# Optimization experiments

Hardware: AMD Instinct MI355X
Metric: run time of the kernel (lower is better)

## Reference

```python
import jax, jax.numpy as jnp
import numpy as np
from jax import lax

B, N, H, L, K = 16, 2000, 128, 3, 5
LN_EPS = 1e-5


def setup_inputs() -> dict:
    key = jax.random.key(0)
    ks = jax.random.split(key, 4)
    node_emb = jax.random.normal(ks[0], (B, N, H), dtype=jnp.float32)
    dist_matrix = jax.random.uniform(ks[1], (B, N, N), dtype=jnp.float32)
    Ws = jax.random.normal(ks[2], (L, H, H), dtype=jnp.float32) / np.sqrt(H)
    bs = jax.random.normal(ks[3], (L, H), dtype=jnp.float32) * 0.02
    gammas = jnp.ones((L, H), dtype=jnp.float32)
    betas = jnp.zeros((L, H), dtype=jnp.float32)
    return {"node_emb": node_emb, "dist_matrix": dist_matrix,
            "Ws": Ws, "bs": bs, "gammas": gammas, "betas": betas}


def _layer_norm(x, gamma, beta):
    mu = jnp.mean(x, axis=-1, keepdims=True)
    var = jnp.mean(jnp.square(x - mu), axis=-1, keepdims=True)
    return (x - mu) * lax.rsqrt(var + LN_EPS) * gamma + beta


def reference(node_emb, dist_matrix, Ws, bs, gammas, betas):
    # kNN mask: k smallest distances per row (B, N, K)
    _, knn_idx = lax.top_k(-dist_matrix, K)
    b_ix = jnp.arange(B)[:, None, None]
    n_ix = jnp.arange(N)[None, :, None]
    knn_mask = jnp.zeros((B, N, N), dtype=bool).at[b_ix, n_ix, knn_idx].set(True)
    scores = jnp.where(knn_mask, -dist_matrix, -jnp.inf)
    weights = jax.nn.softmax(scores, axis=-1)  # (B, N, N)

    h = node_emb
    for l in range(L):
        agg = jnp.einsum('bnm,bmh->bnh', weights, h)
        delta = jax.nn.relu(agg @ Ws[l].T + bs[l])
        h = _layer_norm(h + delta, gammas[l], betas[l])
    return h
```

## Files before the change

### kernel.cpp

```cpp
#include <hip/hip_runtime.h>
#include <hip/hip_bf16.h>

#define BATCH 16
#define NNODE 2000
#define HDIM  128
#define KNN   5
#define NROWS (BATCH * NNODE)
#define LN_EPS 1e-5f

typedef __attribute__((ext_vector_type(8))) short short8;
typedef __attribute__((ext_vector_type(4))) float f32x4;

__device__ __forceinline__ float b2f(short s) {
    unsigned int u = ((unsigned int)(unsigned short)s) << 16;
    return __uint_as_float(u);
}
__device__ __forceinline__ short f2b(float f) {
    __hip_bfloat16 h = __float2bfloat16(f);
    return *reinterpret_cast<short*>(&h);
}

__device__ __forceinline__ unsigned long long pack_di(float v, unsigned int idx) {
    unsigned int b = __float_as_uint(v);
    b = (b & 0x80000000u) ? ~b : (b | 0x80000000u);
    return ((unsigned long long)b << 32) | idx;
}

__global__ __launch_bounds__(256) void knn_prep_kernel(
    const float* __restrict__ dist,
    const float* __restrict__ Ws,
    const float* __restrict__ node_emb,
    __hip_bfloat16* __restrict__ WB,
    short* __restrict__ hb,
    int* __restrict__ w_idx,
    float* __restrict__ w_val)
{
    int tg = blockIdx.x * 256 + threadIdx.x;

    if (tg < 3 * 2048) {
        int l    = tg >> 11;
        int r    = tg & 2047;
        int lane = r & 63;
        int ks   = (r >> 6) & 3;
        int ct   = (r >> 8) & 1;
        int wv   = (r >> 9) & 3;
        int col  = wv * 32 + ct * 16 + (lane & 15);
        int k0   = ks * 32 + (lane >> 4) * 8;
        const float* src = Ws + ((size_t)l << 14) + col * HDIM + k0;
        __hip_bfloat16* dst = WB + ((size_t)tg << 3);
        #pragma unroll
        for (int e = 0; e < 8; ++e) dst[e] = __float2bfloat16(src[e]);
    }

    if (tg < NROWS * HDIM / 8) {
        const float4* src = reinterpret_cast<const float4*>(node_emb) + tg * 2;
        float4 a = src[0], bq = src[1];
        short8 pk;
        pk[0]=f2b(a.x); pk[1]=f2b(a.y); pk[2]=f2b(a.z); pk[3]=f2b(a.w);
        pk[4]=f2b(bq.x); pk[5]=f2b(bq.y); pk[6]=f2b(bq.z); pk[7]=f2b(bq.w);
        *reinterpret_cast<short8*>(hb + (size_t)tg * 8) = pk;
    }

    int row  = blockIdx.x * 4 + (threadIdx.x >> 6);
    int lane = threadIdx.x & 63;
    const float4* r4 = reinterpret_cast<const float4*>(dist + (size_t)row * NNODE);

    unsigned long long pk0 = ~0ull, pk1 = ~0ull, pk2 = ~0ull, pk3 = ~0ull, pk4 = ~0ull;

    auto ins = [&](float d, int m) {
        unsigned long long key = pack_di(d, (unsigned int)m);
        if (key < pk4) {
            pk4 = key;
            unsigned long long t;
            if (pk4 < pk3) { t = pk3; pk3 = pk4; pk4 = t; }
            if (pk3 < pk2) { t = pk2; pk2 = pk3; pk3 = t; }
            if (pk2 < pk1) { t = pk1; pk1 = pk2; pk2 = t; }
            if (pk1 < pk0) { t = pk0; pk0 = pk1; pk1 = t; }
        }
    };

    float4 v[8];
    int base7 = lane + 448;
    bool has8 = base7 < (NNODE / 4);
    #pragma unroll
    for (int i = 0; i < 7; ++i) v[i] = r4[lane + 64 * i];
    v[7] = r4[has8 ? base7 : lane];

    #pragma unroll
    for (int i = 0; i < 7; ++i) {
        int base = (lane + 64 * i) * 4;
        ins(v[i].x, base); ins(v[i].y, base + 1);
        ins(v[i].z, base + 2); ins(v[i].w, base + 3);
    }
    if (has8) {
        int base = base7 * 4;
        ins(v[7].x, base); ins(v[7].y, base + 1);
        ins(v[7].z, base + 2); ins(v[7].w, base + 3);
    }

    unsigned long long chosen[KNN];
    #pragma unroll
    for (int r = 0; r < KNN; ++r) {
        unsigned long long mn = pk0;
        #pragma unroll
        for (int off = 32; off; off >>= 1) {
            unsigned long long o = __shfl_xor(mn, off, 64);
            if (o < mn) mn = o;
        }
        if (pk0 == mn) { pk0 = pk1; pk1 = pk2; pk2 = pk3; pk3 = pk4; pk4 = ~0ull; }
        chosen[r] = mn;
    }

    if (lane == 0) {
        float d[KNN]; int ix[KNN];
        #pragma unroll
        for (int r = 0; r < KNN; ++r) {
            unsigned int ub = (unsigned int)(chosen[r] >> 32);
            ub = (ub & 0x80000000u) ? (ub ^ 0x80000000u) : ~ub;
            d[r]  = __uint_as_float(ub);
            ix[r] = (int)(chosen[r] & 0xffffffffu);
        }
        float e[KNN]; float sum = 0.f;
        #pragma unroll
        for (int r = 0; r < KNN; ++r) { e[r] = expf(d[0] - d[r]); sum += e[r]; }
        float inv = 1.f / sum;
        #pragma unroll
        for (int r = 0; r < KNN; ++r) {
            w_idx[row * KNN + r] = ix[r];
            w_val[row * KNN + r] = e[r] * inv;
        }
    }
}

template<bool OUT_F32>
__global__ __launch_bounds__(256) void layer_kernel_b(
    const short* __restrict__ hin,
    const int*   __restrict__ w_idx,
    const float* __restrict__ w_val,
    const __hip_bfloat16* __restrict__ WB,
    const float* __restrict__ bias,
    const float* __restrict__ gamma,
    const float* __restrict__ beta,
    short* __restrict__ hout_b,
    float* __restrict__ hout_f)
{
    __shared__ __hip_bfloat16 aggb[16][HDIM];
    __shared__ short hown[16][HDIM];
    __shared__ int   sidx[16][KNN];
    __shared__ float sw[16][KNN];
    __shared__ float wred[4][16][2];

    int tid = threadIdx.x;
    int wv  = tid >> 6;
    int l   = tid & 63;

    int bid = blockIdx.x;
    int x   = bid & 7;
    int j   = bid >> 3;
    int hi  = (j >= 125);
    int bsw = 2 * x + hi;
    int gid = bsw * 125 + (j - hi * 125);

    int node0 = gid * 16;
    size_t hbase = (size_t)bsw * NNODE * HDIM;

    const short8* wb = reinterpret_cast<const short8*>(WB);
    short8 bfrag[2][4];
    #pragma unroll
    for (int ct = 0; ct < 2; ++ct)
        #pragma unroll
        for (int ks = 0; ks < 4; ++ks)
            bfrag[ct][ks] = wb[((wv * 2 + ct) * 4 + ks) * 64 + l];

    if (tid < 16 * KNN) {
        int m = tid / KNN, k = tid % KNN;
        sidx[m][k] = w_idx[(node0 + m) * KNN + k];
        sw[m][k]   = w_val[(node0 + m) * KNN + k];
    }
    __syncthreads();

    {
        int m  = tid >> 4;
        int c0 = (tid & 15) * 8;
        short8 own = *reinterpret_cast<const short8*>(
            hin + (size_t)(node0 + m) * HDIM + c0);
        *reinterpret_cast<short8*>(&hown[m][c0]) = own;

        float a0=0,a1=0,a2=0,a3=0,a4=0,a5=0,a6=0,a7=0;
        #pragma unroll
        for (int k = 0; k < KNN; ++k) {
            float wk = sw[m][k];
            short8 hv = *reinterpret_cast<const short8*>(
                hin + hbase + (size_t)sidx[m][k] * HDIM + c0);
            a0 = fmaf(wk, b2f(hv[0]), a0); a1 = fmaf(wk, b2f(hv[1]), a1);
            a2 = fmaf(wk, b2f(hv[2]), a2); a3 = fmaf(wk, b2f(hv[3]), a3);
            a4 = fmaf(wk, b2f(hv[4]), a4); a5 = fmaf(wk, b2f(hv[5]), a5);
            a6 = fmaf(wk, b2f(hv[6]), a6); a7 = fmaf(wk, b2f(hv[7]), a7);
        }
        short8 pk;
        pk[0]=f2b(a0); pk[1]=f2b(a1); pk[2]=f2b(a2); pk[3]=f2b(a3);
        pk[4]=f2b(a4); pk[5]=f2b(a5); pk[6]=f2b(a6); pk[7]=f2b(a7);
        *reinterpret_cast<short8*>(&aggb[tid >> 4][c0]) = pk;
    }
    __syncthreads();

    f32x4 acc0 = {0.f,0.f,0.f,0.f}, acc1 = {0.f,0.f,0.f,0.f};
    #pragma unroll
    for (int ks = 0; ks < 4; ++ks) {
        short8 afrag = *reinterpret_cast<const short8*>(&aggb[l & 15][ks * 32 + (l >> 4) * 8]);
        acc0 = __builtin_amdgcn_mfma_f32_16x16x32_bf16(afrag, bfrag[0][ks], acc0, 0, 0, 0);
        acc1 = __builtin_amdgcn_mfma_f32_16x16x32_bf16(afrag, bfrag[1][ks], acc1, 0, 0, 0);
    }

    int g = l >> 4;
    int col0 = wv * 32 + (l & 15);
    int col1 = col0 + 16;
    float b0  = bias[col0],  b1  = bias[col1];
    float gm0 = gamma[col0], gm1 = gamma[col1];
    float bt0 = beta[col0],  bt1 = beta[col1];

    float y0[4], y1[4];
    #pragma unroll
    for (int r = 0; r < 4; ++r) {
        int rl = g * 4 + r;
        y0[r] = b2f(hown[rl][col0]) + fmaxf(acc0[r] + b0, 0.f);
        y1[r] = b2f(hown[rl][col1]) + fmaxf(acc1[r] + b1, 0.f);
    }

    #pragma unroll
    for (int r = 0; r < 4; ++r) {
        float ss = y0[r] + y1[r];
        float qq = y0[r] * y0[r] + y1[r] * y1[r];
        #pragma unroll
        for (int off = 1; off < 16; off <<= 1) {
            ss += __shfl_xor(ss, off, 64);
            qq += __shfl_xor(qq, off, 64);
        }
        if ((l & 15) == 0) { wred[wv][g * 4 + r][0] = ss; wred[wv][g * 4 + r][1] = qq; }
    }
    __syncthreads();

    #pragma unroll
    for (int r = 0; r < 4; ++r) {
        int row = g * 4 + r;
        float S = wred[0][row][0] + wred[1][row][0] + wred[2][row][0] + wred[3][row][0];
        float Q = wred[0][row][1] + wred[1][row][1] + wred[2][row][1] + wred[3][row][1];
        float mu  = S * (1.f / 128.f);
        float var = Q * (1.f / 128.f) - mu * mu;
        float rs  = rsqrtf(var + LN_EPS);
        size_t orow = (size_t)(node0 + row) * HDIM;
        float o0 = (y0[r] - mu) * rs * gm0 + bt0;
        float o1 = (y1[r] - mu) * rs * gm1 + bt1;
        if (OUT_F32) {
            hout_f[orow + col0] = o0;
            hout_f[orow + col1] = o1;
        } else {
            hout_b[orow + col0] = f2b(o0);
            hout_b[orow + col1] = f2b(o1);
        }
    }
}

extern "C" void kernel_launch(void* const* d_in, const int* in_sizes, int n_in,
                              void* d_out, int out_size, void* d_ws, size_t ws_size,
                              hipStream_t stream) {
    const float* node_emb = (const float*)d_in[0];
    const float* dist     = (const float*)d_in[1];
    const float* Ws       = (const float*)d_in[2];
    const float* bs       = (const float*)d_in[3];
    const float* gammas   = (const float*)d_in[4];
    const float* betas    = (const float*)d_in[5];
    float* out = (float*)d_out;

    char* ws = (char*)d_ws;
    int*   w_idx = (int*)  (ws + 0);
    float* w_val = (float*)(ws + 640000);
    __hip_bfloat16* WB = (__hip_bfloat16*)(ws + 1280000);
    short* hb  = (short*)(ws + 1378304);
    short* h1b = (short*)(ws + 9570304);
    short* h2b = (short*)(ws + 17762304);

    knn_prep_kernel<<<NROWS / 4, 256, 0, stream>>>(
        dist, Ws, node_emb, WB, hb, w_idx, w_val);

    const int nblocks = NROWS / 16;
    const int WL = 16384;

    layer_kernel_b<false><<<nblocks, 256, 0, stream>>>(hb,  w_idx, w_val,
        WB,        bs,          gammas,          betas,          h1b, nullptr);
    layer_kernel_b<false><<<nblocks, 256, 0, stream>>>(h1b, w_idx, w_val,
        WB + WL,   bs + HDIM,   gammas + HDIM,   betas + HDIM,   h2b, nullptr);
    layer_kernel_b<true><<<nblocks, 256, 0, stream>>>(h2b, w_idx, w_val,
        WB + 2*WL, bs + 2*HDIM, gammas + 2*HDIM, betas + 2*HDIM, nullptr, out);
}
```

Measured before the change: 102.3 us.

## Fuse three layer launches into one persistent kernel with grid barrier

Replaces the three per-layer kernel launches with a single persistent kernel of fixed grid size that loops over tiles and synchronises layers through an atomic global barrier. The counters are reset in the prep kernel. This is meant to remove launch overhead and inter-kernel gaps. In exchange it lowers parallelism per layer, adds spin-wait cost, and relies on all blocks being co-resident.

```diff
diff --git a/kernel.cpp b/kernel.cpp
--- a/kernel.cpp
+++ b/kernel.cpp
@@ -6,6 +6,8 @@
 #define HDIM  128
 #define KNN   5
 #define NROWS (BATCH * NNODE)
+#define NTILE (NROWS / 16)
+#define LGRID 768
 #define LN_EPS 1e-5f
 
 typedef __attribute__((ext_vector_type(8))) short short8;
@@ -33,9 +35,15 @@
     __hip_bfloat16* __restrict__ WB,
     short* __restrict__ hb,
     int* __restrict__ w_idx,
-    float* __restrict__ w_val)
+    float* __restrict__ w_val,
+    unsigned int* __restrict__ barrier_ctr)
 {
     int tg = blockIdx.x * 256 + threadIdx.x;
+
+    if (tg < 4) {
+        __hip_atomic_store(&barrier_ctr[tg], 0u, __ATOMIC_RELAXED,
+                           __HIP_MEMORY_SCOPE_AGENT);
+    }
 
     if (tg < 3 * 2048) {
         int l    = tg >> 11;
@@ -132,17 +140,18 @@
     }
 }
 
-template<bool OUT_F32>
-__global__ __launch_bounds__(256) void layer_kernel_b(
-    const short* __restrict__ hin,
+__global__ __launch_bounds__(256, 4) void gcn_layers_kernel(
+    const short* __restrict__ hb,
     const int*   __restrict__ w_idx,
     const float* __restrict__ w_val,
     const __hip_bfloat16* __restrict__ WB,
-    const float* __restrict__ bias,
-    const float* __restrict__ gamma,
-    const float* __restrict__ beta,
-    short* __restrict__ hout_b,
-    float* __restrict__ hout_f)
+    const float* __restrict__ bs,
+    const float* __restrict__ gammas,
+    const float* __restrict__ betas,
+    short* __restrict__ h1b,
+    short* __restrict__ h2b,
+    float* __restrict__ out,
+    unsigned int* __restrict__ barrier_ctr)
 {
     __shared__ __hip_bfloat16 aggb[16][HDIM];
     __shared__ short hown[16][HDIM];
@@ -154,109 +163,132 @@
     int wv  = tid >> 6;
     int l   = tid & 63;
 
-    int bid = blockIdx.x;
-    int x   = bid & 7;
-    int j   = bid >> 3;
-    int hi  = (j >= 125);
-    int bsw = 2 * x + hi;
-    int gid = bsw * 125 + (j - hi * 125);
-
-    int node0 = gid * 16;
-    size_t hbase = (size_t)bsw * NNODE * HDIM;
-
-    const short8* wb = reinterpret_cast<const short8*>(WB);
-    short8 bfrag[2][4];
-    #pragma unroll
-    for (int ct = 0; ct < 2; ++ct)
-        #pragma unroll
-        for (int ks = 0; ks < 4; ++ks)
-            bfrag[ct][ks] = wb[((wv * 2 + ct) * 4 + ks) * 64 + l];
-
-    if (tid < 16 * KNN) {
-        int m = tid / KNN, k = tid % KNN;
-        sidx[m][k] = w_idx[(node0 + m) * KNN + k];
-        sw[m][k]   = w_val[(node0 + m) * KNN + k];
-    }
-    __syncthreads();
-
-    {
-        int m  = tid >> 4;
-        int c0 = (tid & 15) * 8;
-        short8 own = *reinterpret_cast<const short8*>(
-            hin + (size_t)(node0 + m) * HDIM + c0);
-        *reinterpret_cast<short8*>(&hown[m][c0]) = own;
-
-        float a0=0,a1=0,a2=0,a3=0,a4=0,a5=0,a6=0,a7=0;
-        #pragma unroll
-        for (int k = 0; k < KNN; ++k) {
-            float wk = sw[m][k];
-            short8 hv = *reinterpret_cast<const short8*>(
-                hin + hbase + (size_t)sidx[m][k] * HDIM + c0);
-            a0 = fmaf(wk, b2f(hv[0]), a0); a1 = fmaf(wk, b2f(hv[1]), a1);
-            a2 = fmaf(wk, b2f(hv[2]), a2); a3 = fmaf(wk, b2f(hv[3]), a3);
-            a4 = fmaf(wk, b2f(hv[4]), a4); a5 = fmaf(wk, b2f(hv[5]), a5);
-            a6 = fmaf(wk, b2f(hv[6]), a6); a7 = fmaf(wk, b2f(hv[7]), a7);
-        }
-        short8 pk;
-        pk[0]=f2b(a0); pk[1]=f2b(a1); pk[2]=f2b(a2); pk[3]=f2b(a3);
-        pk[4]=f2b(a4); pk[5]=f2b(a5); pk[6]=f2b(a6); pk[7]=f2b(a7);
-        *reinterpret_cast<short8*>(&aggb[tid >> 4][c0]) = pk;
-    }
-    __syncthreads();
-
-    f32x4 acc0 = {0.f,0.f,0.f,0.f}, acc1 = {0.f,0.f,0.f,0.f};
-    #pragma unroll
-    for (int ks = 0; ks < 4; ++ks) {
-        short8 afrag = *reinterpret_cast<const short8*>(&aggb[l & 15][ks * 32 + (l >> 4) * 8]);
-        acc0 = __builtin_amdgcn_mfma_f32_16x16x32_bf16(afrag, bfrag[0][ks], acc0, 0, 0, 0);
-        acc1 = __builtin_amdgcn_mfma_f32_16x16x32_bf16(afrag, bfrag[1][ks], acc1, 0, 0, 0);
-    }
-
-    int g = l >> 4;
-    int col0 = wv * 32 + (l & 15);
-    int col1 = col0 + 16;
-    float b0  = bias[col0],  b1  = bias[col1];
-    float gm0 = gamma[col0], gm1 = gamma[col1];
-    float bt0 = beta[col0],  bt1 = beta[col1];
-
-    float y0[4], y1[4];
-    #pragma unroll
-    for (int r = 0; r < 4; ++r) {
-        int rl = g * 4 + r;
-        y0[r] = b2f(hown[rl][col0]) + fmaxf(acc0[r] + b0, 0.f);
-        y1[r] = b2f(hown[rl][col1]) + fmaxf(acc1[r] + b1, 0.f);
-    }
-
-    #pragma unroll
-    for (int r = 0; r < 4; ++r) {
-        float ss = y0[r] + y1[r];
-        float qq = y0[r] * y0[r] + y1[r] * y1[r];
-        #pragma unroll
-        for (int off = 1; off < 16; off <<= 1) {
-            ss += __shfl_xor(ss, off, 64);
-            qq += __shfl_xor(qq, off, 64);
-        }
-        if ((l & 15) == 0) { wred[wv][g * 4 + r][0] = ss; wred[wv][g * 4 + r][1] = qq; }
-    }
-    __syncthreads();
-
-    #pragma unroll
-    for (int r = 0; r < 4; ++r) {
-        int row = g * 4 + r;
-        float S = wred[0][row][0] + wred[1][row][0] + wred[2][row][0] + wred[3][row][0];
-        float Q = wred[0][row][1] + wred[1][row][1] + wred[2][row][1] + wred[3][row][1];
-        float mu  = S * (1.f / 128.f);
-        float var = Q * (1.f / 128.f) - mu * mu;
-        float rs  = rsqrtf(var + LN_EPS);
-        size_t orow = (size_t)(node0 + row) * HDIM;
-        float o0 = (y0[r] - mu) * rs * gm0 + bt0;
-        float o1 = (y1[r] - mu) * rs * gm1 + bt1;
-        if (OUT_F32) {
-            hout_f[orow + col0] = o0;
-            hout_f[orow + col1] = o1;
-        } else {
-            hout_b[orow + col0] = f2b(o0);
-            hout_b[orow + col1] = f2b(o1);
+    for (int layer = 0; layer < 3; ++layer) {
+        const short* hin = (layer == 0) ? hb : (layer == 1) ? h1b : h2b;
+        short* houtb     = (layer == 0) ? h1b : h2b;
+        const float* bias  = bs     + layer * HDIM;
+        const float* gamma = gammas + layer * HDIM;
+        const float* beta  = betas  + layer * HDIM;
+
+        const short8* wb = reinterpret_cast<const short8*>(WB) + (size_t)layer * 2048;
+        short8 bfrag[2][4];
+        #pragma unroll
+        for (int ct = 0; ct < 2; ++ct)
+            #pragma unroll
+            for (int ks = 0; ks < 4; ++ks)
+                bfrag[ct][ks] = wb[((wv * 2 + ct) * 4 + ks) * 64 + l];
+
+        for (int t = blockIdx.x; t < NTILE; t += LGRID) {
+            int x   = t & 7;
+            int j   = t >> 3;
+            int hi  = (j >= 125);
+            int bsw = 2 * x + hi;
+            int gid = bsw * 125 + (j - hi * 125);
+            int node0 = gid * 16;
+            size_t hbase = (size_t)bsw * NNODE * HDIM;
+
+            if (tid < 16 * KNN) {
+                int m = tid / KNN, k = tid % KNN;
+                sidx[m][k] = w_idx[(node0 + m) * KNN + k];
+                sw[m][k]   = w_val[(node0 + m) * KNN + k];
+            }
+            __syncthreads();
+
+            {
+                int m  = tid >> 4;
+                int c0 = (tid & 15) * 8;
+                short8 own = *reinterpret_cast<const short8*>(
+                    hin + (size_t)(node0 + m) * HDIM + c0);
+                *reinterpret_cast<short8*>(&hown[m][c0]) = own;
+
+                float a0=0,a1=0,a2=0,a3=0,a4=0,a5=0,a6=0,a7=0;
+                #pragma unroll
+                for (int k = 0; k < KNN; ++k) {
+                    float wk = sw[m][k];
+                    short8 hv = *reinterpret_cast<const short8*>(
+                        hin + hbase + (size_t)sidx[m][k] * HDIM + c0);
+                    a0 = fmaf(wk, b2f(hv[0]), a0); a1 = fmaf(wk, b2f(hv[1]), a1);
+                    a2 = fmaf(wk, b2f(hv[2]), a2); a3 = fmaf(wk, b2f(hv[3]), a3);
+                    a4 = fmaf(wk, b2f(hv[4]), a4); a5 = fmaf(wk, b2f(hv[5]), a5);
+                    a6 = fmaf(wk, b2f(hv[6]), a6); a7 = fmaf(wk, b2f(hv[7]), a7);
+                }
+                short8 pk;
+                pk[0]=f2b(a0); pk[1]=f2b(a1); pk[2]=f2b(a2); pk[3]=f2b(a3);
+                pk[4]=f2b(a4); pk[5]=f2b(a5); pk[6]=f2b(a6); pk[7]=f2b(a7);
+                *reinterpret_cast<short8*>(&aggb[m][c0]) = pk;
+            }
+            __syncthreads();
+
+            f32x4 acc0 = {0.f,0.f,0.f,0.f}, acc1 = {0.f,0.f,0.f,0.f};
+            #pragma unroll
+            for (int ks = 0; ks < 4; ++ks) {
+                short8 afrag = *reinterpret_cast<const short8*>(
+                    &aggb[l & 15][ks * 32 + (l >> 4) * 8]);
+                acc0 = __builtin_amdgcn_mfma_f32_16x16x32_bf16(afrag, bfrag[0][ks], acc0, 0, 0, 0);
+                acc1 = __builtin_amdgcn_mfma_f32_16x16x32_bf16(afrag, bfrag[1][ks], acc1, 0, 0, 0);
+            }
+
+            int g = l >> 4;
+            int col0 = wv * 32 + (l & 15);
+            int col1 = col0 + 16;
+            float b0  = bias[col0],  b1  = bias[col1];
+            float gm0 = gamma[col0], gm1 = gamma[col1];
+            float bt0 = beta[col0],  bt1 = beta[col1];
+
+            float y0[4], y1[4];
+            #pragma unroll
+            for (int r = 0; r < 4; ++r) {
+                int rl = g * 4 + r;
+                y0[r] = b2f(hown[rl][col0]) + fmaxf(acc0[r] + b0, 0.f);
+                y1[r] = b2f(hown[rl][col1]) + fmaxf(acc1[r] + b1, 0.f);
+            }
+
+            #pragma unroll
+            for (int r = 0; r < 4; ++r) {
+                float ss = y0[r] + y1[r];
+                float qq = y0[r] * y0[r] + y1[r] * y1[r];
+                #pragma unroll
+                for (int off = 1; off < 16; off <<= 1) {
+                    ss += __shfl_xor(ss, off, 64);
+                    qq += __shfl_xor(qq, off, 64);
+                }
+                if ((l & 15) == 0) { wred[wv][g * 4 + r][0] = ss; wred[wv][g * 4 + r][1] = qq; }
+            }
+            __syncthreads();
+
+            #pragma unroll
+            for (int r = 0; r < 4; ++r) {
+                int row = g * 4 + r;
+                float S = wred[0][row][0] + wred[1][row][0] + wred[2][row][0] + wred[3][row][0];
+                float Q = wred[0][row][1] + wred[1][row][1] + wred[2][row][1] + wred[3][row][1];
+                float mu  = S * (1.f / 128.f);
+                float var = Q * (1.f / 128.f) - mu * mu;
+                float rs  = rsqrtf(var + LN_EPS);
+                size_t orow = (size_t)(node0 + row) * HDIM;
+                float o0 = (y0[r] - mu) * rs * gm0 + bt0;
+                float o1 = (y1[r] - mu) * rs * gm1 + bt1;
+                if (layer == 2) {
+                    out[orow + col0] = o0;
+                    out[orow + col1] = o1;
+                } else {
+                    houtb[orow + col0] = f2b(o0);
+                    houtb[orow + col1] = f2b(o1);
+                }
+            }
+            __syncthreads();
+        }
+
+        if (layer < 2) {
+            __syncthreads();
+            if (tid == 0) {
+                __hip_atomic_fetch_add(&barrier_ctr[layer], 1u,
+                                       __ATOMIC_ACQ_REL, __HIP_MEMORY_SCOPE_AGENT);
+                while (__hip_atomic_load(&barrier_ctr[layer], __ATOMIC_ACQUIRE,
+                                         __HIP_MEMORY_SCOPE_AGENT) < (unsigned)LGRID) {
+                    __builtin_amdgcn_s_sleep(8);
+                }
+            }
+            __syncthreads();
         }
     }
 }
@@ -276,20 +308,14 @@
     int*   w_idx = (int*)  (ws + 0);
     float* w_val = (float*)(ws + 640000);
     __hip_bfloat16* WB = (__hip_bfloat16*)(ws + 1280000);
-    short* hb  = (short*)(ws + 1378304);
-    short* h1b = (short*)(ws + 9570304);
-    short* h2b = (short*)(ws + 17762304);
+    unsigned int* barrier_ctr = (unsigned int*)(ws + 1378304);
+    short* hb  = (short*)(ws + 1378320);
+    short* h1b = (short*)(ws + 9570320);
+    short* h2b = (short*)(ws + 17762320);
 
     knn_prep_kernel<<<NROWS / 4, 256, 0, stream>>>(
-        dist, Ws, node_emb, WB, hb, w_idx, w_val);
-
-    const int nblocks = NROWS / 16;
-    const int WL = 16384;
-
-    layer_kernel_b<false><<<nblocks, 256, 0, stream>>>(hb,  w_idx, w_val,
-        WB,        bs,          gammas,          betas,          h1b, nullptr);
-    layer_kernel_b<false><<<nblocks, 256, 0, stream>>>(h1b, w_idx, w_val,
-        WB + WL,   bs + HDIM,   gammas + HDIM,   betas + HDIM,   h2b, nullptr);
-    layer_kernel_b<true><<<nblocks, 256, 0, stream>>>(h2b, w_idx, w_val,
-        WB + 2*WL, bs + 2*HDIM, gammas + 2*HDIM, betas + 2*HDIM, nullptr, out);
-}
+        dist, Ws, node_emb, WB, hb, w_idx, w_val, barrier_ctr);
+
+    gcn_layers_kernel<<<LGRID, 256, 0, stream>>>(
+        hb, w_idx, w_val, WB, bs, gammas, betas, h1b, h2b, out, barrier_ctr);
+}
```

Result: slower. 266.4 us (+160.4%).

## Fuse kNN selection with first layer's aggregation, GEMM and LayerNorm

Applied to the files above, without the earlier changes.

The kNN/softmax prep kernel now also computes layer 0 for its 4 rows. It gathers neighbours straight from fp32 node_emb, runs the MFMA matmul with Ws converted to bf16 in registers, applies bias, ReLU, residual and LayerNorm, and writes h1 in bf16. This drops the separate bf16 copy of node_emb and one layer launch with its reads and writes. In exchange each 4-row block reads fp32 Ws for every block and runs 16-row MFMAs with only 4 valid rows, which adds L2 traffic and wasted math.

```diff
diff --git a/kernel.cpp b/kernel.cpp
--- a/kernel.cpp
+++ b/kernel.cpp
@@ -26,108 +26,210 @@
     return ((unsigned long long)b << 32) | idx;
 }
 
-__global__ __launch_bounds__(256) void knn_prep_kernel(
+__global__ __launch_bounds__(256) void knn_l0_kernel(
     const float* __restrict__ dist,
+    const float* __restrict__ node_emb,
     const float* __restrict__ Ws,
-    const float* __restrict__ node_emb,
+    const float* __restrict__ bias0,
+    const float* __restrict__ gamma0,
+    const float* __restrict__ beta0,
     __hip_bfloat16* __restrict__ WB,
-    short* __restrict__ hb,
     int* __restrict__ w_idx,
-    float* __restrict__ w_val)
+    float* __restrict__ w_val,
+    short* __restrict__ h1b)
 {
-    int tg = blockIdx.x * 256 + threadIdx.x;
-
-    if (tg < 3 * 2048) {
-        int l    = tg >> 11;
+    __shared__ __hip_bfloat16 aggb[16][HDIM];
+    __shared__ float hown[4][HDIM];
+    __shared__ int   sidx[4][KNN];
+    __shared__ float sw[4][KNN];
+    __shared__ float wred[4][4][2];
+
+    int tid = threadIdx.x;
+    int wv  = tid >> 6;
+    int l   = tid & 63;
+    int bid = blockIdx.x;
+    int row   = bid * 4 + wv;
+    int node0 = bid * 4;
+    int b     = node0 / NNODE;
+    size_t hbase = (size_t)b * NNODE * HDIM;
+
+    {
+        short8 z = {0,0,0,0,0,0,0,0};
+        reinterpret_cast<short8*>(&aggb[0][0])[tid] = z;
+    }
+
+    int tg = bid * 256 + tid;
+    if (tg < 2 * 2048) {
+        int lw   = 1 + (tg >> 11);
         int r    = tg & 2047;
         int lane = r & 63;
         int ks   = (r >> 6) & 3;
         int ct   = (r >> 8) & 1;
-        int wv   = (r >> 9) & 3;
-        int col  = wv * 32 + ct * 16 + (lane & 15);
+        int wvv  = (r >> 9) & 3;
+        int col  = wvv * 32 + ct * 16 + (lane & 15);
         int k0   = ks * 32 + (lane >> 4) * 8;
-        const float* src = Ws + ((size_t)l << 14) + col * HDIM + k0;
+        const float* src = Ws + ((size_t)lw << 14) + col * HDIM + k0;
         __hip_bfloat16* dst = WB + ((size_t)tg << 3);
         #pragma unroll
         for (int e = 0; e < 8; ++e) dst[e] = __float2bfloat16(src[e]);
     }
 
-    if (tg < NROWS * HDIM / 8) {
-        const float4* src = reinterpret_cast<const float4*>(node_emb) + tg * 2;
-        float4 a = src[0], bq = src[1];
-        short8 pk;
-        pk[0]=f2b(a.x); pk[1]=f2b(a.y); pk[2]=f2b(a.z); pk[3]=f2b(a.w);
-        pk[4]=f2b(bq.x); pk[5]=f2b(bq.y); pk[6]=f2b(bq.z); pk[7]=f2b(bq.w);
-        *reinterpret_cast<short8*>(hb + (size_t)tg * 8) = pk;
-    }
-
-    int row  = blockIdx.x * 4 + (threadIdx.x >> 6);
-    int lane = threadIdx.x & 63;
-    const float4* r4 = reinterpret_cast<const float4*>(dist + (size_t)row * NNODE);
-
-    unsigned long long pk0 = ~0ull, pk1 = ~0ull, pk2 = ~0ull, pk3 = ~0ull, pk4 = ~0ull;
-
-    auto ins = [&](float d, int m) {
-        unsigned long long key = pack_di(d, (unsigned int)m);
-        if (key < pk4) {
-            pk4 = key;
-            unsigned long long t;
-            if (pk4 < pk3) { t = pk3; pk3 = pk4; pk4 = t; }
-            if (pk3 < pk2) { t = pk2; pk2 = pk3; pk3 = t; }
-            if (pk2 < pk1) { t = pk1; pk1 = pk2; pk2 = t; }
-            if (pk1 < pk0) { t = pk0; pk0 = pk1; pk1 = t; }
-        }
-    };
-
-    float4 v[8];
-    int base7 = lane + 448;
-    bool has8 = base7 < (NNODE / 4);
-    #pragma unroll
-    for (int i = 0; i < 7; ++i) v[i] = r4[lane + 64 * i];
-    v[7] = r4[has8 ? base7 : lane];
-
-    #pragma unroll
-    for (int i = 0; i < 7; ++i) {
-        int base = (lane + 64 * i) * 4;
-        ins(v[i].x, base); ins(v[i].y, base + 1);
-        ins(v[i].z, base + 2); ins(v[i].w, base + 3);
-    }
-    if (has8) {
-        int base = base7 * 4;
-        ins(v[7].x, base); ins(v[7].y, base + 1);
-        ins(v[7].z, base + 2); ins(v[7].w, base + 3);
-    }
-
-    unsigned long long chosen[KNN];
-    #pragma unroll
-    for (int r = 0; r < KNN; ++r) {
-        unsigned long long mn = pk0;
-        #pragma unroll
-        for (int off = 32; off; off >>= 1) {
-            unsigned long long o = __shfl_xor(mn, off, 64);
-            if (o < mn) mn = o;
-        }
-        if (pk0 == mn) { pk0 = pk1; pk1 = pk2; pk2 = pk3; pk3 = pk4; pk4 = ~0ull; }
-        chosen[r] = mn;
-    }
-
-    if (lane == 0) {
-        float d[KNN]; int ix[KNN];
+    {
+        const float4* r4 = reinterpret_cast<const float4*>(dist + (size_t)row * NNODE);
+        unsigned long long pk0=~0ull, pk1=~0ull, pk2=~0ull, pk3=~0ull, pk4=~0ull;
+
+        auto ins = [&](float d, int m) {
+            unsigned long long key = pack_di(d, (unsigned int)m);
+            if (key < pk4) {
+                pk4 = key;
+                unsigned long long t;
+                if (pk4 < pk3) { t = pk3; pk3 = pk4; pk4 = t; }
+                if (pk3 < pk2) { t = pk2; pk2 = pk3; pk3 = t; }
+                if (pk2 < pk1) { t = pk1; pk1 = pk2; pk2 = t; }
+                if (pk1 < pk0) { t = pk0; pk0 = pk1; pk1 = t; }
+            }
+        };
+
+        float4 v[8];
+        int base7 = l + 448;
+        bool has8 = base7 < (NNODE / 4);
+        #pragma unroll
+        for (int i = 0; i < 7; ++i) v[i] = r4[l + 64 * i];
+        v[7] = r4[has8 ? base7 : l];
+
+        #pragma unroll
+        for (int i = 0; i < 7; ++i) {
+            int base = (l + 64 * i) * 4;
+            ins(v[i].x, base); ins(v[i].y, base + 1);
+            ins(v[i].z, base + 2); ins(v[i].w, base + 3);
+        }
+        if (has8) {
+            int base = base7 * 4;
+            ins(v[7].x, base); ins(v[7].y, base + 1);
+            ins(v[7].z, base + 2); ins(v[7].w, base + 3);
+        }
+
+        unsigned long long chosen[KNN];
         #pragma unroll
         for (int r = 0; r < KNN; ++r) {
-            unsigned int ub = (unsigned int)(chosen[r] >> 32);
-            ub = (ub & 0x80000000u) ? (ub ^ 0x80000000u) : ~ub;
-            d[r]  = __uint_as_float(ub);
-            ix[r] = (int)(chosen[r] & 0xffffffffu);
-        }
-        float e[KNN]; float sum = 0.f;
-        #pragma unroll
-        for (int r = 0; r < KNN; ++r) { e[r] = expf(d[0] - d[r]); sum += e[r]; }
-        float inv = 1.f / sum;
-        #pragma unroll
-        for (int r = 0; r < KNN; ++r) {
-            w_idx[row * KNN + r] = ix[r];
-            w_val[row * KNN + r] = e[r] * inv;
+            unsigned long long mn = pk0;
+            #pragma unroll
+            for (int off = 32; off; off >>= 1) {
+                unsigned long long o = __shfl_xor(mn, off, 64);
+                if (o < mn) mn = o;
+            }
+            if (pk0 == mn) { pk0 = pk1; pk1 = pk2; pk2 = pk3; pk3 = pk4; pk4 = ~0ull; }
+            chosen[r] = mn;
+        }
+
+        if (l == 0) {
+            float d[KNN]; int ix[KNN];
+            #pragma unroll
+            for (int r = 0; r < KNN; ++r) {
+                unsigned int ub = (unsigned int)(chosen[r] >> 32);
+                ub = (ub & 0x80000000u) ? (ub ^ 0x80000000u) : ~ub;
+                d[r]  = __uint_as_float(ub);
+                ix[r] = (int)(chosen[r] & 0xffffffffu);
+            }
+            float e[KNN]; float sum = 0.f;
+            #pragma unroll
+            for (int r = 0; r < KNN; ++r) { e[r] = expf(d[0] - d[r]); sum += e[r]; }
+            float inv = 1.f / sum;
+            #pragma unroll
+            for (int r = 0; r < KNN; ++r) {
+                float wt = e[r] * inv;
+                sidx[wv][r] = ix[r];
+                sw[wv][r]   = wt;
+                w_idx[row * KNN + r] = ix[r];
+                w_val[row * KNN + r] = wt;
+            }
+        }
+    }
+    __syncthreads();
+
+    {
+        int c = 2 * l;
+        float2 ow = *reinterpret_cast<const float2*>(
+            node_emb + (size_t)row * HDIM + c);
+        *reinterpret_cast<float2*>(&hown[wv][c]) = ow;
+
+        float a0 = 0.f, a1 = 0.f;
+        #pragma unroll
+        for (int k = 0; k < KNN; ++k) {
+            float wk = sw[wv][k];
+            float2 hv = *reinterpret_cast<const float2*>(
+                node_emb + hbase + (size_t)sidx[wv][k] * HDIM + c);
+            a0 = fmaf(wk, hv.x, a0);
+            a1 = fmaf(wk, hv.y, a1);
+        }
+        unsigned short u0 = (unsigned short)f2b(a0);
+        unsigned short u1 = (unsigned short)f2b(a1);
+        *reinterpret_cast<ushort2*>(&aggb[wv][c]) = make_ushort2(u0, u1);
+    }
+
+    short8 bfrag[2][4];
+    #pragma unroll
+    for (int ct = 0; ct < 2; ++ct) {
+        int col = wv * 32 + ct * 16 + (l & 15);
+        const float* wp = Ws + col * HDIM + (l >> 4) * 8;
+        #pragma unroll
+        for (int ks = 0; ks < 4; ++ks) {
+            float4 u0 = *reinterpret_cast<const float4*>(wp + ks * 32);
+            float4 u1 = *reinterpret_cast<const float4*>(wp + ks * 32 + 4);
+            short8 rfr;
+            rfr[0]=f2b(u0.x); rfr[1]=f2b(u0.y); rfr[2]=f2b(u0.z); rfr[3]=f2b(u0.w);
+            rfr[4]=f2b(u1.x); rfr[5]=f2b(u1.y); rfr[6]=f2b(u1.z); rfr[7]=f2b(u1.w);
+            bfrag[ct][ks] = rfr;
+        }
+    }
+    __syncthreads();
+
+    f32x4 acc0 = {0.f,0.f,0.f,0.f}, acc1 = {0.f,0.f,0.f,0.f};
+    #pragma unroll
+    for (int ks = 0; ks < 4; ++ks) {
+        short8 afrag = *reinterpret_cast<const short8*>(
+            &aggb[l & 15][ks * 32 + (l >> 4) * 8]);
+        acc0 = __builtin_amdgcn_mfma_f32_16x16x32_bf16(afrag, bfrag[0][ks], acc0, 0, 0, 0);
+        acc1 = __builtin_amdgcn_mfma_f32_16x16x32_bf16(afrag, bfrag[1][ks], acc1, 0, 0, 0);
+    }
+
+    float y0[4], y1[4];
+    int col0 = wv * 32 + (l & 15);
+    int col1 = col0 + 16;
+    if (l < 16) {
+        float b0  = bias0[col0],  b1  = bias0[col1];
+        #pragma unroll
+        for (int r = 0; r < 4; ++r) {
+            y0[r] = hown[r][col0] + fmaxf(acc0[r] + b0, 0.f);
+            y1[r] = hown[r][col1] + fmaxf(acc1[r] + b1, 0.f);
+        }
+        #pragma unroll
+        for (int r = 0; r < 4; ++r) {
+            float ss = y0[r] + y1[r];
+            float qq = y0[r] * y0[r] + y1[r] * y1[r];
+            #pragma unroll
+            for (int off = 1; off < 16; off <<= 1) {
+                ss += __shfl_xor(ss, off, 64);
+                qq += __shfl_xor(qq, off, 64);
+            }
+            if (l == 0) { wred[wv][r][0] = ss; wred[wv][r][1] = qq; }
+        }
+    }
+    __syncthreads();
+
+    if (l < 16) {
+        float gm0 = gamma0[col0], gm1 = gamma0[col1];
+        float bt0 = beta0[col0],  bt1 = beta0[col1];
+        #pragma unroll
+        for (int r = 0; r < 4; ++r) {
+            float S = wred[0][r][0] + wred[1][r][0] + wred[2][r][0] + wred[3][r][0];
+            float Q = wred[0][r][1] + wred[1][r][1] + wred[2][r][1] + wred[3][r][1];
+            float mu  = S * (1.f / 128.f);
+            float var = Q * (1.f / 128.f) - mu * mu;
+            float rs  = rsqrtf(var + LN_EPS);
+            size_t orow = (size_t)(node0 + r) * HDIM;
+            h1b[orow + col0] = f2b((y0[r] - mu) * rs * gm0 + bt0);
+            h1b[orow + col1] = f2b((y1[r] - mu) * rs * gm1 + bt1);
         }
     }
 }
@@ -200,7 +302,7 @@
         short8 pk;
         pk[0]=f2b(a0); pk[1]=f2b(a1); pk[2]=f2b(a2); pk[3]=f2b(a3);
         pk[4]=f2b(a4); pk[5]=f2b(a5); pk[6]=f2b(a6); pk[7]=f2b(a7);
-        *reinterpret_cast<short8*>(&aggb[tid >> 4][c0]) = pk;
+        *reinterpret_cast<short8*>(&aggb[m][c0]) = pk;
     }
     __syncthreads();
 
@@ -276,20 +378,16 @@
     int*   w_idx = (int*)  (ws + 0);
     float* w_val = (float*)(ws + 640000);
     __hip_bfloat16* WB = (__hip_bfloat16*)(ws + 1280000);
-    short* hb  = (short*)(ws + 1378304);
-    short* h1b = (short*)(ws + 9570304);
-    short* h2b = (short*)(ws + 17762304);
-
-    knn_prep_kernel<<<NROWS / 4, 256, 0, stream>>>(
-        dist, Ws, node_emb, WB, hb, w_idx, w_val);
+    short* h1b = (short*)(ws + 1345536);
+    short* h2b = (short*)(ws + 9537536);
+
+    knn_l0_kernel<<<NROWS / 4, 256, 0, stream>>>(
+        dist, node_emb, Ws, bs, gammas, betas, WB, w_idx, w_val, h1b);
 
     const int nblocks = NROWS / 16;
-    const int WL = 16384;
-
-    layer_kernel_b<false><<<nblocks, 256, 0, stream>>>(hb,  w_idx, w_val,
-        WB,        bs,          gammas,          betas,          h1b, nullptr);
+
     layer_kernel_b<false><<<nblocks, 256, 0, stream>>>(h1b, w_idx, w_val,
-        WB + WL,   bs + HDIM,   gammas + HDIM,   betas + HDIM,   h2b, nullptr);
+        WB,          bs + HDIM,    gammas + HDIM,    betas + HDIM,    h2b, nullptr);
     layer_kernel_b<true><<<nblocks, 256, 0, stream>>>(h2b, w_idx, w_val,
-        WB + 2*WL, bs + 2*HDIM, gammas + 2*HDIM, betas + 2*HDIM, nullptr, out);
-}
+        WB + 16384,  bs + 2*HDIM,  gammas + 2*HDIM,  betas + 2*HDIM,  nullptr, out);
+}
```

After: 125.4 us. 22.6% more time.
